# Kernel tuning notes

Hardware: AMD Instinct MI355X
Metric: run time of the kernel (lower is better)

## Reference

```python
import jax, jax.numpy as jnp
import numpy as np

B, L, D = 32, 2048, 64
MASK_FILL = -1.0e6  # matches torch code's -1000000.0


def setup_inputs() -> dict:
    key = jax.random.key(0)
    kq, kk, kv, kl = jax.random.split(key, 4)
    queries = jax.random.normal(kq, (B, L, D), dtype=jnp.float32)
    keys = jax.random.normal(kk, (B, L, D), dtype=jnp.float32)
    values = jax.random.normal(kv, (B, L, D), dtype=jnp.float32)
    valid_lens = jax.random.randint(kl, (B,), 1, L + 1, dtype=jnp.int64)
    return {"queries": queries, "keys": keys, "values": values,
            "valid_lens": valid_lens}


def reference(queries, keys, values, valid_lens):
    d = queries.shape[-1]
    # [B, Lq, Lk] scores
    scores = jnp.einsum('bqd,bkd->bqk', queries, keys) / jnp.sqrt(
        jnp.asarray(d, dtype=queries.dtype))
    # length mask: position k valid iff k < valid_lens[b]
    Lk = scores.shape[-1]
    mask = jnp.arange(Lk)[None, :] < valid_lens[:, None]      # [B, Lk]
    scores = jnp.where(mask[:, None, :], scores, MASK_FILL)   # broadcast over Lq
    attn = jax.nn.softmax(scores, axis=-1)
    # dropout p=0.0 -> identity
    return jnp.einsum('bqk,bkv->bqv', attn, values)
```

## Files before the change

kernel.cpp:

```cpp
#include <hip/hip_runtime.h>
#include <hip/hip_bf16.h>
#include <math.h>


#define BB 32
#define LL 2048
#define DD 64
#define QBLK 64
#define KBLK 64
#define NTILES (BB * (LL / QBLK))
#define GRID 768

typedef __attribute__((ext_vector_type(8))) short bf16x8;
typedef __attribute__((ext_vector_type(4))) float f32x4;

static __device__ __forceinline__ short f2bf(float f) {
    __hip_bfloat16 h = __float2bfloat16(f);
    return *reinterpret_cast<short*>(&h);
}
static __device__ __forceinline__ unsigned pk2(float a, float b) {
    return (unsigned)(unsigned short)f2bf(a) | ((unsigned)(unsigned short)f2bf(b) << 16);
}
static __device__ __forceinline__ float exp2c(float x) {
    return __builtin_amdgcn_exp2f(x);
}
static __device__ __forceinline__ int kswz(int row) { return (row & 7) << 3; }
static __device__ __forceinline__ int vswz(int d)   { return ((d ^ (d >> 2)) & 7) << 3; }
static __device__ __forceinline__ int pswz(int row) { return (((row & 7) ^ (row >> 3)) & 7) << 3; }

__global__ void init_ctr_kernel(const int* __restrict__ vlen, int* __restrict__ ws) {
    int t = threadIdx.x;
    if (t == 0) ws[0] = 0;
    if (t < BB) {
        int v = vlen[t];
        int rank = 0;
        for (int j = 0; j < BB; ++j) {
            int vj = vlen[j];
            rank += (vj > v) || (vj == v && j < t);
        }
        ws[1 + rank] = t;
    }
}

__global__ __launch_bounds__(256, 2) void attn_mfma_kernel(
    const float* __restrict__ Q, const float* __restrict__ K,
    const float* __restrict__ V, const int* __restrict__ vlen,
    float* __restrict__ O, int* __restrict__ ws)
{
    __shared__ __align__(16) short Ks[KBLK * DD];
    __shared__ __align__(16) short Vt[DD * KBLK];
    __shared__ __align__(16) short Pl[4 * 16 * KBLK];
    __shared__ int s_tile;

    int* ctr = ws;
    const int* order = ws + 1;

    const int tid  = threadIdx.x;
    const int wid  = tid >> 6;
    const int lane = tid & 63;
    const int lq   = lane & 15;
    const int lg   = lane >> 4;

    const int vd4 = (tid & 15) * 4;
    const int vkr = (tid >> 4) * 4;

    const float QSCALE = 0.125f * 1.44269504088896341f;

    for (;;) {
        __syncthreads();
        if (tid == 0) s_tile = atomicAdd(ctr, 1);
        __syncthreads();
        const int tile = s_tile;
        if (tile >= NTILES) break;

        const int b     = order[tile >> 5];
        const int qt    = tile & 31;
        const int qbase = qt * QBLK + wid * 16;
        const int valid = vlen[b];

        bf16x8 qf[2];
        {
            const float* Qr = Q + ((size_t)b * LL + qbase + lq) * DD;
            #pragma unroll
            for (int ds_ = 0; ds_ < 2; ++ds_) {
                const float4* p4 = reinterpret_cast<const float4*>(Qr + ds_ * 32 + lg * 8);
                float4 a = p4[0], c = p4[1];
                bf16x8 f;
                f[0] = f2bf(a.x * QSCALE); f[1] = f2bf(a.y * QSCALE);
                f[2] = f2bf(a.z * QSCALE); f[3] = f2bf(a.w * QSCALE);
                f[4] = f2bf(c.x * QSCALE); f[5] = f2bf(c.y * QSCALE);
                f[6] = f2bf(c.z * QSCALE); f[7] = f2bf(c.w * QSCALE);
                qf[ds_] = f;
            }
        }

        f32x4 acc[4];
        #pragma unroll
        for (int n = 0; n < 4; ++n) acc[n] = (f32x4){0.f, 0.f, 0.f, 0.f};
        float m_ = -1e30f, l_ = 0.f;

        const int ntiles = (valid + KBLK - 1) / KBLK;
        const float4* Kg4 = reinterpret_cast<const float4*>(K + (size_t)b * LL * DD);
        const float4* Vg4 = reinterpret_cast<const float4*>(V + (size_t)b * LL * DD);

        float4 kpre[4], vpre[4];
        #pragma unroll
        for (int i = 0; i < 4; ++i) kpre[i] = Kg4[tid + i * 256];
        #pragma unroll
        for (int r = 0; r < 4; ++r) vpre[r] = Vg4[(vkr + r) * 16 + (tid & 15)];

        for (int kt = 0; kt < ntiles; ++kt) {
            __syncthreads();

            #pragma unroll
            for (int i = 0; i < 4; ++i) {
                int idx = tid + i * 256;
                int kr  = idx >> 4;
                int dc  = (idx & 15) * 4;
                float4 kv = kpre[i];
                int e = (kr * 64 + dc) ^ kswz(kr);
                *reinterpret_cast<uint2*>(&Ks[e]) =
                    make_uint2(pk2(kv.x, kv.y), pk2(kv.z, kv.w));
            }
            {
                float4 v0 = vpre[0], v1 = vpre[1], v2 = vpre[2], v3 = vpre[3];
                int e0 = ((vd4 + 0) * 64 + vkr) ^ vswz(vd4 + 0);
                *reinterpret_cast<uint2*>(&Vt[e0]) = make_uint2(pk2(v0.x, v1.x), pk2(v2.x, v3.x));
                int e1 = ((vd4 + 1) * 64 + vkr) ^ vswz(vd4 + 1);
                *reinterpret_cast<uint2*>(&Vt[e1]) = make_uint2(pk2(v0.y, v1.y), pk2(v2.y, v3.y));
                int e2 = ((vd4 + 2) * 64 + vkr) ^ vswz(vd4 + 2);
                *reinterpret_cast<uint2*>(&Vt[e2]) = make_uint2(pk2(v0.z, v1.z), pk2(v2.z, v3.z));
                int e3 = ((vd4 + 3) * 64 + vkr) ^ vswz(vd4 + 3);
                *reinterpret_cast<uint2*>(&Vt[e3]) = make_uint2(pk2(v0.w, v1.w), pk2(v2.w, v3.w));
            }
            __syncthreads();

            if (kt + 1 < ntiles) {
                const int base4 = (kt + 1) * KBLK * (DD / 4);
                #pragma unroll
                for (int i = 0; i < 4; ++i) kpre[i] = Kg4[base4 + tid + i * 256];
                #pragma unroll
                for (int r = 0; r < 4; ++r) vpre[r] = Vg4[base4 + (vkr + r) * 16 + (tid & 15)];
            }

            f32x4 s[4];
            #pragma unroll
            for (int t = 0; t < 4; ++t) {
                f32x4 a = (f32x4){0.f, 0.f, 0.f, 0.f};
                const int krow = t * 16 + lq;
                #pragma unroll
                for (int ds_ = 0; ds_ < 2; ++ds_) {
                    int e = (krow * 64 + ds_ * 32 + lg * 8) ^ kswz(krow);
                    bf16x8 kf = *reinterpret_cast<const bf16x8*>(&Ks[e]);
                    a = __builtin_amdgcn_mfma_f32_16x16x32_bf16(kf, qf[ds_], a, 0, 0, 0);
                }
                s[t] = a;
            }

            const bool tail = (kt == ntiles - 1) && (valid & (KBLK - 1));
            if (tail) {
                #pragma unroll
                for (int t = 0; t < 4; ++t)
                    #pragma unroll
                    for (int r = 0; r < 4; ++r) {
                        int kg = kt * KBLK + t * 16 + lg * 4 + r;
                        if (kg >= valid) s[t][r] = -1e30f;
                    }
            }
            float mx = s[0][0];
            #pragma unroll
            for (int t = 0; t < 4; ++t)
                #pragma unroll
                for (int r = 0; r < 4; ++r) mx = fmaxf(mx, s[t][r]);
            mx = fmaxf(mx, __shfl_xor(mx, 16, 64));
            mx = fmaxf(mx, __shfl_xor(mx, 32, 64));

            if (__any(mx - m_ > 8.0f)) {
                float mnew = fmaxf(m_, mx);
                float corr = exp2c(m_ - mnew);
                m_ = mnew;
                l_ *= corr;
                #pragma unroll
                for (int r = 0; r < 4; ++r) {
                    float cq = __shfl(corr, lg * 4 + r, 64);
                    #pragma unroll
                    for (int n = 0; n < 4; ++n) acc[n][r] *= cq;
                }
            }

            float ls = 0.f;
            #pragma unroll
            for (int t = 0; t < 4; ++t)
                #pragma unroll
                for (int r = 0; r < 4; ++r) {
                    float p = exp2c(s[t][r] - m_);
                    s[t][r] = p;
                    ls += p;
                }
            ls += __shfl_xor(ls, 16, 64);
            ls += __shfl_xor(ls, 32, 64);
            l_ += ls;

            short* Pw = &Pl[wid * (16 * KBLK)];
            #pragma unroll
            for (int t = 0; t < 4; ++t) {
                int e = (lq * 64 + t * 16 + lg * 4) ^ pswz(lq);
                *reinterpret_cast<uint2*>(&Pw[e]) =
                    make_uint2(pk2(s[t][0], s[t][1]), pk2(s[t][2], s[t][3]));
            }

            #pragma unroll
            for (int ks_ = 0; ks_ < 2; ++ks_) {
                int pe = (lq * 64 + ks_ * 32 + lg * 8) ^ pswz(lq);
                bf16x8 pf = *reinterpret_cast<const bf16x8*>(&Pw[pe]);
                #pragma unroll
                for (int n = 0; n < 4; ++n) {
                    int drow = n * 16 + lq;
                    int ve = (drow * 64 + ks_ * 32 + lg * 8) ^ vswz(drow);
                    bf16x8 vf = *reinterpret_cast<const bf16x8*>(&Vt[ve]);
                    acc[n] = __builtin_amdgcn_mfma_f32_16x16x32_bf16(pf, vf, acc[n], 0, 0, 0);
                }
            }
        }

        float linv[4];
        #pragma unroll
        for (int r = 0; r < 4; ++r)
            linv[r] = 1.f / __shfl(l_, lg * 4 + r, 64);
        float* Ob = O + ((size_t)b * LL + qbase) * DD;
        #pragma unroll
        for (int n = 0; n < 4; ++n) {
            #pragma unroll
            for (int r = 0; r < 4; ++r) {
                Ob[(size_t)(lg * 4 + r) * DD + n * 16 + lq] = acc[n][r] * linv[r];
            }
        }
    }
}

extern "C" void kernel_launch(void* const* d_in, const int* in_sizes, int n_in,
                              void* d_out, int out_size, void* d_ws, size_t ws_size,
                              hipStream_t stream) {
    const float* Q = (const float*)d_in[0];
    const float* K = (const float*)d_in[1];
    const float* V = (const float*)d_in[2];
    const int* vlen = (const int*)d_in[3];
    float* O = (float*)d_out;
    int* ws = (int*)d_ws;

    init_ctr_kernel<<<1, 64, 0, stream>>>(vlen, ws);
    attn_mfma_kernel<<<GRID, 256, 0, stream>>>(Q, K, V, vlen, O, ws);
}
```

Baseline: 71.85 us.

## Double-buffer K/V shared tiles and halve per-wave P staging buffer

Adds two LDS buffers for K and V so the next tile is staged while the current one is consumed, which cuts the two barriers per iteration to one. Global prefetch now runs two tiles ahead. The P scratch per wave shrinks to 16x32 and is written and read one half at a time without swizzling, which removes some LDS footprint but may add bank conflicts. Total LDS use grows because of the doubled K/V buffers, which could limit occupancy.

```diff
diff --git a/kernel.cpp b/kernel.cpp
--- a/kernel.cpp
+++ b/kernel.cpp
@@ -26,7 +26,6 @@
 }
 static __device__ __forceinline__ int kswz(int row) { return (row & 7) << 3; }
 static __device__ __forceinline__ int vswz(int d)   { return ((d ^ (d >> 2)) & 7) << 3; }
-static __device__ __forceinline__ int pswz(int row) { return (((row & 7) ^ (row >> 3)) & 7) << 3; }
 
 __global__ void init_ctr_kernel(const int* __restrict__ vlen, int* __restrict__ ws) {
     int t = threadIdx.x;
@@ -47,9 +46,9 @@
     const float* __restrict__ V, const int* __restrict__ vlen,
     float* __restrict__ O, int* __restrict__ ws)
 {
-    __shared__ __align__(16) short Ks[KBLK * DD];
-    __shared__ __align__(16) short Vt[DD * KBLK];
-    __shared__ __align__(16) short Pl[4 * 16 * KBLK];
+    __shared__ __align__(16) short Ks[2][KBLK * DD];
+    __shared__ __align__(16) short Vt[2][DD * KBLK];
+    __shared__ __align__(16) short Pl[4][16 * 32];
     __shared__ int s_tile;
 
     int* ctr = ws;
@@ -65,6 +64,8 @@
     const int vkr = (tid >> 4) * 4;
 
     const float QSCALE = 0.125f * 1.44269504088896341f;
+
+    float4 kpre[4], vpre[4];
 
     for (;;) {
         __syncthreads();
@@ -77,6 +78,41 @@
         const int qt    = tile & 31;
         const int qbase = qt * QBLK + wid * 16;
         const int valid = vlen[b];
+        const int ntiles = (valid + KBLK - 1) / KBLK;
+
+        const float4* Kg4 = reinterpret_cast<const float4*>(K + (size_t)b * LL * DD);
+        const float4* Vg4 = reinterpret_cast<const float4*>(V + (size_t)b * LL * DD);
+
+        auto prefetch = [&](int t) {
+            const int base4 = t * KBLK * (DD / 4);
+            #pragma unroll
+            for (int i = 0; i < 4; ++i) kpre[i] = Kg4[base4 + tid + i * 256];
+            #pragma unroll
+            for (int r = 0; r < 4; ++r) vpre[r] = Vg4[base4 + (vkr + r) * 16 + (tid & 15)];
+        };
+        auto stage = [&](int buf) {
+            short* ks = &Ks[buf][0];
+            short* vt = &Vt[buf][0];
+            #pragma unroll
+            for (int i = 0; i < 4; ++i) {
+                int idx = tid + i * 256;
+                int kr  = idx >> 4;
+                int dc  = (idx & 15) * 4;
+                float4 kv = kpre[i];
+                int e = (kr * 64 + dc) ^ kswz(kr);
+                *reinterpret_cast<uint2*>(&ks[e]) =
+                    make_uint2(pk2(kv.x, kv.y), pk2(kv.z, kv.w));
+            }
+            float4 v0 = vpre[0], v1 = vpre[1], v2 = vpre[2], v3 = vpre[3];
+            int e0 = ((vd4 + 0) * 64 + vkr) ^ vswz(vd4 + 0);
+            *reinterpret_cast<uint2*>(&vt[e0]) = make_uint2(pk2(v0.x, v1.x), pk2(v2.x, v3.x));
+            int e1 = ((vd4 + 1) * 64 + vkr) ^ vswz(vd4 + 1);
+            *reinterpret_cast<uint2*>(&vt[e1]) = make_uint2(pk2(v0.y, v1.y), pk2(v2.y, v3.y));
+            int e2 = ((vd4 + 2) * 64 + vkr) ^ vswz(vd4 + 2);
+            *reinterpret_cast<uint2*>(&vt[e2]) = make_uint2(pk2(v0.z, v1.z), pk2(v2.z, v3.z));
+            int e3 = ((vd4 + 3) * 64 + vkr) ^ vswz(vd4 + 3);
+            *reinterpret_cast<uint2*>(&vt[e3]) = make_uint2(pk2(v0.w, v1.w), pk2(v2.w, v3.w));
+        };
 
         bf16x8 qf[2];
         {
@@ -99,50 +135,20 @@
         for (int n = 0; n < 4; ++n) acc[n] = (f32x4){0.f, 0.f, 0.f, 0.f};
         float m_ = -1e30f, l_ = 0.f;
 
-        const int ntiles = (valid + KBLK - 1) / KBLK;
-        const float4* Kg4 = reinterpret_cast<const float4*>(K + (size_t)b * LL * DD);
-        const float4* Vg4 = reinterpret_cast<const float4*>(V + (size_t)b * LL * DD);
-
-        float4 kpre[4], vpre[4];
-        #pragma unroll
-        for (int i = 0; i < 4; ++i) kpre[i] = Kg4[tid + i * 256];
-        #pragma unroll
-        for (int r = 0; r < 4; ++r) vpre[r] = Vg4[(vkr + r) * 16 + (tid & 15)];
+        prefetch(0);
+        stage(0);
+        if (ntiles > 1) prefetch(1);
+        __syncthreads();
 
         for (int kt = 0; kt < ntiles; ++kt) {
-            __syncthreads();
-
-            #pragma unroll
-            for (int i = 0; i < 4; ++i) {
-                int idx = tid + i * 256;
-                int kr  = idx >> 4;
-                int dc  = (idx & 15) * 4;
-                float4 kv = kpre[i];
-                int e = (kr * 64 + dc) ^ kswz(kr);
-                *reinterpret_cast<uint2*>(&Ks[e]) =
-                    make_uint2(pk2(kv.x, kv.y), pk2(kv.z, kv.w));
-            }
-            {
-                float4 v0 = vpre[0], v1 = vpre[1], v2 = vpre[2], v3 = vpre[3];
-                int e0 = ((vd4 + 0) * 64 + vkr) ^ vswz(vd4 + 0);
-                *reinterpret_cast<uint2*>(&Vt[e0]) = make_uint2(pk2(v0.x, v1.x), pk2(v2.x, v3.x));
-                int e1 = ((vd4 + 1) * 64 + vkr) ^ vswz(vd4 + 1);
-                *reinterpret_cast<uint2*>(&Vt[e1]) = make_uint2(pk2(v0.y, v1.y), pk2(v2.y, v3.y));
-                int e2 = ((vd4 + 2) * 64 + vkr) ^ vswz(vd4 + 2);
-                *reinterpret_cast<uint2*>(&Vt[e2]) = make_uint2(pk2(v0.z, v1.z), pk2(v2.z, v3.z));
-                int e3 = ((vd4 + 3) * 64 + vkr) ^ vswz(vd4 + 3);
-                *reinterpret_cast<uint2*>(&Vt[e3]) = make_uint2(pk2(v0.w, v1.w), pk2(v2.w, v3.w));
-            }
-            __syncthreads();
+            const int cur = kt & 1;
 
             if (kt + 1 < ntiles) {
-                const int base4 = (kt + 1) * KBLK * (DD / 4);
-                #pragma unroll
-                for (int i = 0; i < 4; ++i) kpre[i] = Kg4[base4 + tid + i * 256];
-                #pragma unroll
-                for (int r = 0; r < 4; ++r) vpre[r] = Vg4[base4 + (vkr + r) * 16 + (tid & 15)];
-            }
-
+                stage(cur ^ 1);
+                if (kt + 2 < ntiles) prefetch(kt + 2);
+            }
+
+            const short* ks = &Ks[cur][0];
             f32x4 s[4];
             #pragma unroll
             for (int t = 0; t < 4; ++t) {
@@ -151,7 +157,7 @@
                 #pragma unroll
                 for (int ds_ = 0; ds_ < 2; ++ds_) {
                     int e = (krow * 64 + ds_ * 32 + lg * 8) ^ kswz(krow);
-                    bf16x8 kf = *reinterpret_cast<const bf16x8*>(&Ks[e]);
+                    bf16x8 kf = *reinterpret_cast<const bf16x8*>(&ks[e]);
                     a = __builtin_amdgcn_mfma_f32_16x16x32_bf16(kf, qf[ds_], a, 0, 0, 0);
                 }
                 s[t] = a;
@@ -201,26 +207,28 @@
             ls += __shfl_xor(ls, 32, 64);
             l_ += ls;
 
-            short* Pw = &Pl[wid * (16 * KBLK)];
-            #pragma unroll
-            for (int t = 0; t < 4; ++t) {
-                int e = (lq * 64 + t * 16 + lg * 4) ^ pswz(lq);
-                *reinterpret_cast<uint2*>(&Pw[e]) =
-                    make_uint2(pk2(s[t][0], s[t][1]), pk2(s[t][2], s[t][3]));
-            }
-
-            #pragma unroll
-            for (int ks_ = 0; ks_ < 2; ++ks_) {
-                int pe = (lq * 64 + ks_ * 32 + lg * 8) ^ pswz(lq);
-                bf16x8 pf = *reinterpret_cast<const bf16x8*>(&Pw[pe]);
+            const short* vt = &Vt[cur][0];
+            short* Pw = &Pl[wid][0];
+            #pragma unroll
+            for (int c = 0; c < 2; ++c) {
+                #pragma unroll
+                for (int th = 0; th < 2; ++th) {
+                    int t = 2 * c + th;
+                    int e = lq * 32 + th * 16 + lg * 4;
+                    *reinterpret_cast<uint2*>(&Pw[e]) =
+                        make_uint2(pk2(s[t][0], s[t][1]), pk2(s[t][2], s[t][3]));
+                }
+                bf16x8 pf = *reinterpret_cast<const bf16x8*>(&Pw[lq * 32 + lg * 8]);
                 #pragma unroll
                 for (int n = 0; n < 4; ++n) {
                     int drow = n * 16 + lq;
-                    int ve = (drow * 64 + ks_ * 32 + lg * 8) ^ vswz(drow);
-                    bf16x8 vf = *reinterpret_cast<const bf16x8*>(&Vt[ve]);
+                    int ve = (drow * 64 + c * 32 + lg * 8) ^ vswz(drow);
+                    bf16x8 vf = *reinterpret_cast<const bf16x8*>(&vt[ve]);
                     acc[n] = __builtin_amdgcn_mfma_f32_16x16x32_bf16(pf, vf, acc[n], 0, 0, 0);
                 }
             }
+
+            __syncthreads();
         }
 
         float linv[4];
```

Result: slower. 77.24 us (+7.5%).

## Pre-convert K/V to swizzled bf16 images and stream tiles via direct LDS loads

Applied to the files above, without the earlier changes.

Adds a pre-pass kernel that converts K and V to bf16 once, already swizzled and transposed into the LDS tile layout, and stores the result in workspace. The attention kernel then copies each tile straight into double-buffered LDS with global_load_lds, prefetching the next tile during compute. This removes the fp32-to-bf16 conversion and transposition that every query tile repeated, and halves the bytes fetched per tile. In exchange it adds an extra kernel launch plus a write and read of the bf16 image, and doubles LDS use, which may lower occupancy.

```diff
diff --git a/kernel.cpp b/kernel.cpp
--- a/kernel.cpp
+++ b/kernel.cpp
@@ -27,6 +27,18 @@
 static __device__ __forceinline__ int kswz(int row) { return (row & 7) << 3; }
 static __device__ __forceinline__ int vswz(int d)   { return ((d ^ (d >> 2)) & 7) << 3; }
 static __device__ __forceinline__ int pswz(int row) { return (((row & 7) ^ (row >> 3)) & 7) << 3; }
+
+static __device__ __forceinline__ void cp16(const unsigned short* g,
+                                            unsigned short* lbase, int lane) {
+#if __has_builtin(__builtin_amdgcn_global_load_lds)
+    __builtin_amdgcn_global_load_lds(
+        (__attribute__((address_space(1))) void*)g,
+        (__attribute__((address_space(3))) void*)lbase, 16, 0, 0);
+#else
+    *reinterpret_cast<uint4*>(lbase + lane * 8) =
+        *reinterpret_cast<const uint4*>(g);
+#endif
+}
 
 __global__ void init_ctr_kernel(const int* __restrict__ vlen, int* __restrict__ ws) {
     int t = threadIdx.x;
@@ -42,14 +54,54 @@
     }
 }
 
+__global__ __launch_bounds__(256) void convert_kv_kernel(
+    const float* __restrict__ K, const float* __restrict__ V,
+    unsigned short* __restrict__ kv)
+{
+    const int tile = blockIdx.x;
+    const int tid  = threadIdx.x;
+    const float*  Kt  = K + (size_t)tile * (KBLK * DD);
+    const float4* Vg4 = reinterpret_cast<const float4*>(V + (size_t)tile * (KBLK * DD));
+    unsigned short* img = kv + (size_t)tile * 8192;
+
+    #pragma unroll
+    for (int g = 0; g < 2; ++g) {
+        int gi = tid + g * 256;
+        int kr = gi >> 3;
+        int dc = ((gi & 7) * 8) ^ kswz(kr);
+        const float4* src = reinterpret_cast<const float4*>(Kt + kr * DD + dc);
+        float4 a = src[0], c = src[1];
+        uint4 w;
+        w.x = pk2(a.x, a.y); w.y = pk2(a.z, a.w);
+        w.z = pk2(c.x, c.y); w.w = pk2(c.z, c.w);
+        *reinterpret_cast<uint4*>(img + (size_t)gi * 8) = w;
+    }
+
+    unsigned short* img2 = img + 4096;
+    const int vd4 = (tid & 15) * 4;
+    const int vkr = (tid >> 4) * 4;
+    float4 v0 = Vg4[(vkr + 0) * 16 + (tid & 15)];
+    float4 v1 = Vg4[(vkr + 1) * 16 + (tid & 15)];
+    float4 v2 = Vg4[(vkr + 2) * 16 + (tid & 15)];
+    float4 v3 = Vg4[(vkr + 3) * 16 + (tid & 15)];
+    int e0 = ((vd4 + 0) * 64 + vkr) ^ vswz(vd4 + 0);
+    *reinterpret_cast<uint2*>(img2 + e0) = make_uint2(pk2(v0.x, v1.x), pk2(v2.x, v3.x));
+    int e1 = ((vd4 + 1) * 64 + vkr) ^ vswz(vd4 + 1);
+    *reinterpret_cast<uint2*>(img2 + e1) = make_uint2(pk2(v0.y, v1.y), pk2(v2.y, v3.y));
+    int e2 = ((vd4 + 2) * 64 + vkr) ^ vswz(vd4 + 2);
+    *reinterpret_cast<uint2*>(img2 + e2) = make_uint2(pk2(v0.z, v1.z), pk2(v2.z, v3.z));
+    int e3 = ((vd4 + 3) * 64 + vkr) ^ vswz(vd4 + 3);
+    *reinterpret_cast<uint2*>(img2 + e3) = make_uint2(pk2(v0.w, v1.w), pk2(v2.w, v3.w));
+}
+
 __global__ __launch_bounds__(256, 2) void attn_mfma_kernel(
-    const float* __restrict__ Q, const float* __restrict__ K,
-    const float* __restrict__ V, const int* __restrict__ vlen,
+    const float* __restrict__ Q, const int* __restrict__ vlen,
+    const unsigned short* __restrict__ kvimg,
     float* __restrict__ O, int* __restrict__ ws)
 {
-    __shared__ __align__(16) short Ks[KBLK * DD];
-    __shared__ __align__(16) short Vt[DD * KBLK];
-    __shared__ __align__(16) short Pl[4 * 16 * KBLK];
+    __shared__ __align__(16) unsigned short Ks[2][KBLK * DD];
+    __shared__ __align__(16) unsigned short Vt[2][KBLK * DD];
+    __shared__ __align__(16) unsigned short Pl[4][16 * KBLK];
     __shared__ int s_tile;
 
     int* ctr = ws;
@@ -60,9 +112,6 @@
     const int lane = tid & 63;
     const int lq   = lane & 15;
     const int lg   = lane >> 4;
-
-    const int vd4 = (tid & 15) * 4;
-    const int vkr = (tid >> 4) * 4;
 
     const float QSCALE = 0.125f * 1.44269504088896341f;
 
@@ -77,6 +126,17 @@
         const int qt    = tile & 31;
         const int qbase = qt * QBLK + wid * 16;
         const int valid = vlen[b];
+        const int ntiles = (valid + KBLK - 1) / KBLK;
+
+        const unsigned short* tbase = kvimg + (size_t)b * (32 * 8192);
+
+        auto load_tile = [&](int t, int buf) {
+            const unsigned short* tp = tbase + (size_t)t * 8192 + wid * 512 + lane * 8;
+            cp16(tp,        &Ks[buf][wid * 512],        lane);
+            cp16(tp + 2048, &Ks[buf][2048 + wid * 512], lane);
+            cp16(tp + 4096, &Vt[buf][wid * 512],        lane);
+            cp16(tp + 6144, &Vt[buf][2048 + wid * 512], lane);
+        };
 
         bf16x8 qf[2];
         {
@@ -99,50 +159,15 @@
         for (int n = 0; n < 4; ++n) acc[n] = (f32x4){0.f, 0.f, 0.f, 0.f};
         float m_ = -1e30f, l_ = 0.f;
 
-        const int ntiles = (valid + KBLK - 1) / KBLK;
-        const float4* Kg4 = reinterpret_cast<const float4*>(K + (size_t)b * LL * DD);
-        const float4* Vg4 = reinterpret_cast<const float4*>(V + (size_t)b * LL * DD);
-
-        float4 kpre[4], vpre[4];
-        #pragma unroll
-        for (int i = 0; i < 4; ++i) kpre[i] = Kg4[tid + i * 256];
-        #pragma unroll
-        for (int r = 0; r < 4; ++r) vpre[r] = Vg4[(vkr + r) * 16 + (tid & 15)];
+        load_tile(0, 0);
+        __syncthreads();
 
         for (int kt = 0; kt < ntiles; ++kt) {
-            __syncthreads();
-
-            #pragma unroll
-            for (int i = 0; i < 4; ++i) {
-                int idx = tid + i * 256;
-                int kr  = idx >> 4;
-                int dc  = (idx & 15) * 4;
-                float4 kv = kpre[i];
-                int e = (kr * 64 + dc) ^ kswz(kr);
-                *reinterpret_cast<uint2*>(&Ks[e]) =
-                    make_uint2(pk2(kv.x, kv.y), pk2(kv.z, kv.w));
-            }
-            {
-                float4 v0 = vpre[0], v1 = vpre[1], v2 = vpre[2], v3 = vpre[3];
-                int e0 = ((vd4 + 0) * 64 + vkr) ^ vswz(vd4 + 0);
-                *reinterpret_cast<uint2*>(&Vt[e0]) = make_uint2(pk2(v0.x, v1.x), pk2(v2.x, v3.x));
-                int e1 = ((vd4 + 1) * 64 + vkr) ^ vswz(vd4 + 1);
-                *reinterpret_cast<uint2*>(&Vt[e1]) = make_uint2(pk2(v0.y, v1.y), pk2(v2.y, v3.y));
-                int e2 = ((vd4 + 2) * 64 + vkr) ^ vswz(vd4 + 2);
-                *reinterpret_cast<uint2*>(&Vt[e2]) = make_uint2(pk2(v0.z, v1.z), pk2(v2.z, v3.z));
-                int e3 = ((vd4 + 3) * 64 + vkr) ^ vswz(vd4 + 3);
-                *reinterpret_cast<uint2*>(&Vt[e3]) = make_uint2(pk2(v0.w, v1.w), pk2(v2.w, v3.w));
-            }
-            __syncthreads();
-
-            if (kt + 1 < ntiles) {
-                const int base4 = (kt + 1) * KBLK * (DD / 4);
-                #pragma unroll
-                for (int i = 0; i < 4; ++i) kpre[i] = Kg4[base4 + tid + i * 256];
-                #pragma unroll
-                for (int r = 0; r < 4; ++r) vpre[r] = Vg4[base4 + (vkr + r) * 16 + (tid & 15)];
-            }
-
+            const int cur = kt & 1;
+
+            if (kt + 1 < ntiles) load_tile(kt + 1, cur ^ 1);
+
+            const unsigned short* ks = &Ks[cur][0];
             f32x4 s[4];
             #pragma unroll
             for (int t = 0; t < 4; ++t) {
@@ -151,7 +176,7 @@
                 #pragma unroll
                 for (int ds_ = 0; ds_ < 2; ++ds_) {
                     int e = (krow * 64 + ds_ * 32 + lg * 8) ^ kswz(krow);
-                    bf16x8 kf = *reinterpret_cast<const bf16x8*>(&Ks[e]);
+                    bf16x8 kf = *reinterpret_cast<const bf16x8*>(&ks[e]);
                     a = __builtin_amdgcn_mfma_f32_16x16x32_bf16(kf, qf[ds_], a, 0, 0, 0);
                 }
                 s[t] = a;
@@ -201,7 +226,7 @@
             ls += __shfl_xor(ls, 32, 64);
             l_ += ls;
 
-            short* Pw = &Pl[wid * (16 * KBLK)];
+            unsigned short* Pw = &Pl[wid][0];
             #pragma unroll
             for (int t = 0; t < 4; ++t) {
                 int e = (lq * 64 + t * 16 + lg * 4) ^ pswz(lq);
@@ -209,6 +234,7 @@
                     make_uint2(pk2(s[t][0], s[t][1]), pk2(s[t][2], s[t][3]));
             }
 
+            const unsigned short* vt = &Vt[cur][0];
             #pragma unroll
             for (int ks_ = 0; ks_ < 2; ++ks_) {
                 int pe = (lq * 64 + ks_ * 32 + lg * 8) ^ pswz(lq);
@@ -217,10 +243,12 @@
                 for (int n = 0; n < 4; ++n) {
                     int drow = n * 16 + lq;
                     int ve = (drow * 64 + ks_ * 32 + lg * 8) ^ vswz(drow);
-                    bf16x8 vf = *reinterpret_cast<const bf16x8*>(&Vt[ve]);
+                    bf16x8 vf = *reinterpret_cast<const bf16x8*>(&vt[ve]);
                     acc[n] = __builtin_amdgcn_mfma_f32_16x16x32_bf16(pf, vf, acc[n], 0, 0, 0);
                 }
             }
+
+            __syncthreads();
         }
 
         float linv[4];
@@ -246,8 +274,11 @@
     const float* V = (const float*)d_in[2];
     const int* vlen = (const int*)d_in[3];
     float* O = (float*)d_out;
-    int* ws = (int*)d_ws;
-
-    init_ctr_kernel<<<1, 64, 0, stream>>>(vlen, ws);
-    attn_mfma_kernel<<<GRID, 256, 0, stream>>>(Q, K, V, vlen, O, ws);
-}
+
+    int* ws_i = (int*)d_ws;
+    unsigned short* kvimg = (unsigned short*)((char*)d_ws + 1024);
+
+    init_ctr_kernel<<<1, 64, 0, stream>>>(vlen, ws_i);
+    convert_kv_kernel<<<BB * (LL / KBLK), 256, 0, stream>>>(K, V, kvimg);
+    attn_mfma_kernel<<<GRID, 256, 0, stream>>>(Q, vlen, kvimg, O, ws_i);
+}
```

Measured after the change: 74.38 us. +3.5%, slower.
